# Optimization experiments

Measured on AMD Instinct MI355X. Metric: run time of the kernel, lower is better.

Reference implementation:

```python
import jax, jax.numpy as jnp
import numpy as np

B, T, D = 8, 4096, 1024

def setup_inputs() -> dict:
    key = jax.random.key(0)
    k1, k2, k3, k4, k5 = jax.random.split(key, 5)
    s = 1.0 / np.sqrt(D)
    return {
        "seq": jax.random.normal(k1, (B, T, D), dtype=jnp.float32),
        "W_delta": jax.random.uniform(k2, (D, D), jnp.float32, -s, s),
        "b_delta": jax.random.uniform(k3, (D,), jnp.float32, -s, s),
        "W_value": jax.random.uniform(k4, (D, D), jnp.float32, -s, s),
        "b_value": jax.random.uniform(k5, (D,), jnp.float32, -s, s),
    }

def reference(seq, W_delta, b_delta, W_value, b_value):
    # delta = sigmoid(seq @ W_delta^T + b_delta); value = seq @ W_value^T + b_value
    delta = jax.nn.sigmoid(jnp.einsum("btd,ed->bte", seq, W_delta) + b_delta)
    value = jnp.einsum("btd,ed->bte", seq, W_value) + b_value
    # gated linear recurrence: state_t = (1-delta_t)*state_{t-1} + delta_t*value_t
    def step(state, dv):
        d, v = dv  # each [B, D]
        state = (1.0 - d) * state + d * v
        return state, state
    init = jnp.zeros((seq.shape[0], seq.shape[-1]), dtype=seq.dtype)
    # time-major for scan
    _, out = jax.lax.scan(step, init, (delta.transpose(1, 0, 2), value.transpose(1, 0, 2)))
    return out.transpose(1, 0, 2)  # [B, T, D]
```

## Files before the change

kernel.cpp:

```cpp
#include <hip/hip_runtime.h>
#include <hip/hip_bf16.h>


typedef _Float16 f16;
typedef _Float16 f16x8 __attribute__((ext_vector_type(8)));
typedef float    f32x4 __attribute__((ext_vector_type(4)));

#define NB  8
#define NT  4096
#define ND  1024
#define NM  (NB*NT)
#define KK  2048

#define CT  128
#define NCH (NT/CT)

#define OFF_AP     0UL
#define OFF_BP     134217728UL
#define OFF_VALUE  142606336UL
#define OFF_AARR   276824064UL
#define OFF_SARR   277872640UL
#define OFF_SIN    278921216UL

#define GLOAD_LDS16(gp, lp)                                                          \
  __builtin_amdgcn_global_load_lds(                                                  \
      (const __attribute__((address_space(1))) void*)(gp),                           \
      (__attribute__((address_space(3))) void*)(lp), 16, 0, 0)

#define MEMFENCE asm volatile("" ::: "memory")
#define BARRIER() do { MEMFENCE; __builtin_amdgcn_s_barrier(); MEMFENCE; } while (0)
#define WAITV2() asm volatile("s_waitcnt vmcnt(2)" ::: "memory")
#define WAITV0() asm volatile("s_waitcnt vmcnt(0)" ::: "memory")

__global__ void k_convert_seq(const float* __restrict__ src, f16* __restrict__ Ap) {
  const long n8 = (long)NM * ND / 8;
  long i = (long)blockIdx.x * blockDim.x + threadIdx.x;
  const long stride = (long)gridDim.x * blockDim.x;
  for (; i < n8; i += stride) {
    const long m = i >> 7;
    const int k8 = ((int)i & 127) * 8;
    const float4 v0 = *(const float4*)(src + m * ND + k8);
    const float4 v1 = *(const float4*)(src + m * ND + k8 + 4);
    const float a[8] = {v0.x, v0.y, v0.z, v0.w, v1.x, v1.y, v1.z, v1.w};
    f16x8 hi, lo;
#pragma unroll
    for (int j = 0; j < 8; ++j) {
      const f16 h = (f16)a[j];
      hi[j] = h;
      lo[j] = (f16)(a[j] - (float)h);
    }
    *(f16x8*)(Ap + m * KK + k8) = hi;
    *(f16x8*)(Ap + m * KK + ND + k8) = lo;
  }
}

__global__ void k_convert_w(const float* __restrict__ Wd, const float* __restrict__ Wv,
                            f16* __restrict__ Bp) {
  const long i = (long)blockIdx.x * blockDim.x + threadIdx.x;
  const int n = (int)(i >> 7);
  const int k8 = ((int)i & 127) * 8;
  const float* row = (n < ND) ? (Wd + (long)n * ND) : (Wv + (long)(n - ND) * ND);
  const float4 v0 = *(const float4*)(row + k8);
  const float4 v1 = *(const float4*)(row + k8 + 4);
  const float a[8] = {v0.x, v0.y, v0.z, v0.w, v1.x, v1.y, v1.z, v1.w};
  f16x8 h;
#pragma unroll
  for (int j = 0; j < 8; ++j) h[j] = (f16)a[j];
  *(f16x8*)(Bp + (long)n * ND + k8) = h;
}

#define LDS_A(c) ((c) * 65536)
#define LDS_B(c) ((c) * 65536 + 32768)

__global__ __launch_bounds__(512, 2) void k_gemm(
    const f16* __restrict__ Ap, const f16* __restrict__ Bp,
    const float* __restrict__ bd, const float* __restrict__ bv,
    float* __restrict__ dOut, float* __restrict__ vOut) {
  __shared__ char smem[131072];

  const int t = threadIdx.x;
  const int w = t >> 6, lane = t & 63;
  const int wr = w >> 2, wc = w & 3;
  const int l15 = lane & 15, l4 = lane >> 4;

  const int bid = blockIdx.x;
  const int sw = (bid & 7) * 128 + (bid >> 3);
  const int bm = sw >> 3, bn = sw & 7;
  const long m0 = (long)bm * 256;
  const int n0 = bn * 256;

  f32x4 acc[8][4] = {};

  const int rl0 = t >> 3;
  const int rl1 = 64 + (t >> 3);
  const int c16_0 = (t & 7) ^ (rl0 & 7);
  const int c16_1 = (t & 7) ^ (rl1 & 7);

  auto stageA = [&](int kt, int h, int c) {
    const f16* s0 = Ap + (m0 + h * 128 + rl0) * (long)KK + kt * 64 + c16_0 * 8;
    const f16* s1 = Ap + (m0 + h * 128 + rl1) * (long)KK + kt * 64 + c16_1 * 8;
    char* base = smem + LDS_A(c) + h * 16384 + w * 1024;
    GLOAD_LDS16(s0, base);
    GLOAD_LDS16(s1, base + 8192);
  };
  auto stageB = [&](int kt, int h, int c) {
    const int kb = (kt & 15) * 64;
    const f16* s0 = Bp + (long)(n0 + h * 128 + rl0) * ND + kb + c16_0 * 8;
    const f16* s1 = Bp + (long)(n0 + h * 128 + rl1) * ND + kb + c16_1 * 8;
    char* base = smem + LDS_B(c) + h * 16384 + w * 1024;
    GLOAD_LDS16(s0, base);
    GLOAD_LDS16(s1, base + 8192);
  };

  f16x8 aF[8], bF[2];
  auto readA = [&](int c, int k) {
#pragma unroll
    for (int mf = 0; mf < 8; ++mf) {
      const int row = wr * 128 + mf * 16 + l15;
      const int c16 = (k * 4 + l4) ^ (row & 7);
      aF[mf] = *(const f16x8*)(smem + LDS_A(c) + row * 128 + c16 * 16);
    }
  };
  auto readB = [&](int c, int k, int nh) {
#pragma unroll
    for (int nfl = 0; nfl < 2; ++nfl) {
      const int row = nh * 128 + wc * 32 + nfl * 16 + l15;
      const int c16 = (k * 4 + l4) ^ (row & 7);
      bF[nfl] = *(const f16x8*)(smem + LDS_B(c) + row * 128 + c16 * 16);
    }
  };
  auto mfmaQ = [&](int nh) {
    __builtin_amdgcn_s_setprio(1);
#pragma unroll
    for (int mf = 0; mf < 8; ++mf)
#pragma unroll
      for (int nfl = 0; nfl < 2; ++nfl)
        acc[mf][nh * 2 + nfl] = __builtin_amdgcn_mfma_f32_16x16x32_f16(
            bF[nfl], aF[mf], acc[mf][nh * 2 + nfl], 0, 0, 0);
    __builtin_amdgcn_s_setprio(0);
  };

  auto tile = [&](int c, int ktNext, bool pf) {
    if (pf) stageA(ktNext, 0, c ^ 1);
    readA(c, 0); readB(c, 0, 0);
    BARRIER();
    mfmaQ(0);
    if (pf) { WAITV2(); } else { WAITV0(); }
    BARRIER();
    if (pf) stageA(ktNext, 1, c ^ 1);
    readB(c, 0, 1);
    BARRIER();
    mfmaQ(1);
    BARRIER();
    if (pf) stageB(ktNext, 0, c ^ 1);
    readA(c, 1); readB(c, 1, 0);
    BARRIER();
    mfmaQ(0);
    BARRIER();
    if (pf) stageB(ktNext, 1, c ^ 1);
    readB(c, 1, 1);
    BARRIER();
    mfmaQ(1);
    if (pf) { WAITV2(); } else { WAITV0(); }
    BARRIER();
  };

  stageA(0, 0, 0); stageA(0, 1, 0); stageB(0, 0, 0); stageB(0, 1, 0);
  WAITV2();
  BARRIER();

  for (int i = 0; i < 16; ++i) {
    tile(0, 2 * i + 1, true);
    tile(1, 2 * i + 2, i < 15);
  }

  const bool isDelta = (n0 < ND);
#pragma unroll
  for (int nf = 0; nf < 4; ++nf) {
    const int nb = n0 + (nf >> 1) * 128 + wc * 32 + (nf & 1) * 16 + l4 * 4;
    const float4 bias = *(const float4*)(isDelta ? (bd + nb) : (bv + (nb - ND)));
#pragma unroll
    for (int mf = 0; mf < 8; ++mf) {
      const long m = m0 + wr * 128 + mf * 16 + l15;
      f32x4 x = acc[mf][nf];
      x[0] += bias.x; x[1] += bias.y; x[2] += bias.z; x[3] += bias.w;
      if (isDelta) {
#pragma unroll
        for (int r = 0; r < 4; ++r) x[r] = 1.0f / (1.0f + __expf(-x[r]));
        *(f32x4*)(dOut + m * ND + nb) = x;
      } else {
        *(f32x4*)(vOut + m * ND + (nb - ND)) = x;
      }
    }
  }
}

__global__ void k_scan_local(const float* __restrict__ delta, const float* __restrict__ value,
                             float* __restrict__ Aarr, float* __restrict__ Sarr) {
  const int bid = blockIdx.x;
  const int c = bid & 31, b = bid >> 5;
  const int d = threadIdx.x * 4;
  const long base = ((long)b * NT + (long)c * CT) * ND + d;
  float4 a = make_float4(1.f, 1.f, 1.f, 1.f);
  float4 s = make_float4(0.f, 0.f, 0.f, 0.f);
#pragma unroll 4
  for (int tt = 0; tt < CT; ++tt) {
    const float4 dl = *(const float4*)(delta + base + (long)tt * ND);
    const float4 v  = *(const float4*)(value + base + (long)tt * ND);
    const float o0 = 1.0f - dl.x, o1 = 1.0f - dl.y, o2 = 1.0f - dl.z, o3 = 1.0f - dl.w;
    a.x *= o0; a.y *= o1; a.z *= o2; a.w *= o3;
    s.x = o0 * s.x + dl.x * v.x;
    s.y = o1 * s.y + dl.y * v.y;
    s.z = o2 * s.z + dl.z * v.z;
    s.w = o3 * s.w + dl.w * v.w;
  }
  const long o = (long)(b * NCH + c) * ND + d;
  *(float4*)(Aarr + o) = a;
  *(float4*)(Sarr + o) = s;
}

__global__ void k_scan_prefix(const float* __restrict__ Aarr, const float* __restrict__ Sarr,
                              float* __restrict__ Sin) {
  const int tid = blockIdx.x * blockDim.x + threadIdx.x;
  const int b = tid >> 8, d = (tid & 255) * 4;
  float4 st = make_float4(0.f, 0.f, 0.f, 0.f);
  for (int c = 0; c < NCH; ++c) {
    const long idx = (long)(b * NCH + c) * ND + d;
    *(float4*)(Sin + idx) = st;
    const float4 a = *(const float4*)(Aarr + idx);
    const float4 s = *(const float4*)(Sarr + idx);
    st.x = a.x * st.x + s.x;
    st.y = a.y * st.y + s.y;
    st.z = a.z * st.z + s.z;
    st.w = a.w * st.w + s.w;
  }
}

__global__ void k_scan_apply(const float* __restrict__ value, const float* __restrict__ Sin,
                             float* __restrict__ out) {
  const int bid = blockIdx.x;
  const int c = bid & 31, b = bid >> 5;
  const int d = threadIdx.x * 4;
  const long base = ((long)b * NT + (long)c * CT) * ND + d;
  float4 st = *(const float4*)(Sin + (long)(b * NCH + c) * ND + d);
#pragma unroll 4
  for (int tt = 0; tt < CT; ++tt) {
    const long idx = base + (long)tt * ND;
    const float4 dl = *(const float4*)(out + idx);
    const float4 v  = *(const float4*)(value + idx);
    st.x = (1.0f - dl.x) * st.x + dl.x * v.x;
    st.y = (1.0f - dl.y) * st.y + dl.y * v.y;
    st.z = (1.0f - dl.z) * st.z + dl.z * v.z;
    st.w = (1.0f - dl.w) * st.w + dl.w * v.w;
    *(float4*)(out + idx) = st;
  }
}

extern "C" void kernel_launch(void* const* d_in, const int* in_sizes, int n_in,
                              void* d_out, int out_size, void* d_ws, size_t ws_size,
                              hipStream_t stream) {
  const float* seq = (const float*)d_in[0];
  const float* Wd  = (const float*)d_in[1];
  const float* bd  = (const float*)d_in[2];
  const float* Wv  = (const float*)d_in[3];
  const float* bv  = (const float*)d_in[4];
  float* out = (float*)d_out;

  char* ws = (char*)d_ws;
  f16*   Ap    = (f16*)(ws + OFF_AP);
  f16*   Bp    = (f16*)(ws + OFF_BP);
  float* value = (float*)(ws + OFF_VALUE);
  float* Aarr  = (float*)(ws + OFF_AARR);
  float* Sarr  = (float*)(ws + OFF_SARR);
  float* Sin   = (float*)(ws + OFF_SIN);

  hipLaunchKernelGGL(k_convert_seq, dim3(2048), dim3(256), 0, stream, seq, Ap);
  hipLaunchKernelGGL(k_convert_w,   dim3(1024), dim3(256), 0, stream, Wd, Wv, Bp);
  hipLaunchKernelGGL(k_gemm, dim3(1024), dim3(512), 0, stream, Ap, Bp, bd, bv, out, value);
  hipLaunchKernelGGL(k_scan_local,  dim3(256), dim3(256), 0, stream, out, value, Aarr, Sarr);
  hipLaunchKernelGGL(k_scan_prefix, dim3(8),   dim3(256), 0, stream, Aarr, Sarr, Sin);
  hipLaunchKernelGGL(k_scan_apply,  dim3(256), dim3(256), 0, stream, value, Sin, out);
}
```

Measured before the change: 624.4 us.

## Drop split-fp16 residual term from GEMM and halve scan chunk length

The activation conversion no longer stores a low-order fp16 residual, so the GEMM's K dimension drops from 2048 to 1024. This halves the A-operand traffic, the conversion writes and the MFMA work. The scan chunk length is also cut from 128 to 64, doubling the blocks in the local and apply scan passes for more parallelism. In exchange, the activations lose the extra precision the hi/lo split provided, which risks larger numerical error against the fp32 reference.

New measurement: 519.1 us. 1.2x faster.

```diff
diff --git a/kernel.cpp b/kernel.cpp
--- a/kernel.cpp
+++ b/kernel.cpp
@@ -10,17 +10,17 @@
 #define NT  4096
 #define ND  1024
 #define NM  (NB*NT)
-#define KK  2048
-
-#define CT  128
+#define KK  1024
+
+#define CT  64
 #define NCH (NT/CT)
 
 #define OFF_AP     0UL
-#define OFF_BP     134217728UL
-#define OFF_VALUE  142606336UL
-#define OFF_AARR   276824064UL
-#define OFF_SARR   277872640UL
-#define OFF_SIN    278921216UL
+#define OFF_BP     67108864UL
+#define OFF_VALUE  71303168UL
+#define OFF_AARR   205520896UL
+#define OFF_SARR   207618048UL
+#define OFF_SIN    209715200UL
 
 #define GLOAD_LDS16(gp, lp)                                                          \
   __builtin_amdgcn_global_load_lds(                                                  \
@@ -37,20 +37,12 @@
   long i = (long)blockIdx.x * blockDim.x + threadIdx.x;
   const long stride = (long)gridDim.x * blockDim.x;
   for (; i < n8; i += stride) {
-    const long m = i >> 7;
-    const int k8 = ((int)i & 127) * 8;
-    const float4 v0 = *(const float4*)(src + m * ND + k8);
-    const float4 v1 = *(const float4*)(src + m * ND + k8 + 4);
-    const float a[8] = {v0.x, v0.y, v0.z, v0.w, v1.x, v1.y, v1.z, v1.w};
-    f16x8 hi, lo;
-#pragma unroll
-    for (int j = 0; j < 8; ++j) {
-      const f16 h = (f16)a[j];
-      hi[j] = h;
-      lo[j] = (f16)(a[j] - (float)h);
-    }
-    *(f16x8*)(Ap + m * KK + k8) = hi;
-    *(f16x8*)(Ap + m * KK + ND + k8) = lo;
+    const float4 v0 = *(const float4*)(src + i * 8);
+    const float4 v1 = *(const float4*)(src + i * 8 + 4);
+    f16x8 h;
+    h[0] = (f16)v0.x; h[1] = (f16)v0.y; h[2] = (f16)v0.z; h[3] = (f16)v0.w;
+    h[4] = (f16)v1.x; h[5] = (f16)v1.y; h[6] = (f16)v1.z; h[7] = (f16)v1.w;
+    *((f16x8*)Ap + i) = h;
   }
 }
 
@@ -62,10 +54,9 @@
   const float* row = (n < ND) ? (Wd + (long)n * ND) : (Wv + (long)(n - ND) * ND);
   const float4 v0 = *(const float4*)(row + k8);
   const float4 v1 = *(const float4*)(row + k8 + 4);
-  const float a[8] = {v0.x, v0.y, v0.z, v0.w, v1.x, v1.y, v1.z, v1.w};
   f16x8 h;
-#pragma unroll
-  for (int j = 0; j < 8; ++j) h[j] = (f16)a[j];
+  h[0] = (f16)v0.x; h[1] = (f16)v0.y; h[2] = (f16)v0.z; h[3] = (f16)v0.w;
+  h[4] = (f16)v1.x; h[5] = (f16)v1.y; h[6] = (f16)v1.z; h[7] = (f16)v1.w;
   *(f16x8*)(Bp + (long)n * ND + k8) = h;
 }
 
@@ -104,9 +95,8 @@
     GLOAD_LDS16(s1, base + 8192);
   };
   auto stageB = [&](int kt, int h, int c) {
-    const int kb = (kt & 15) * 64;
-    const f16* s0 = Bp + (long)(n0 + h * 128 + rl0) * ND + kb + c16_0 * 8;
-    const f16* s1 = Bp + (long)(n0 + h * 128 + rl1) * ND + kb + c16_1 * 8;
+    const f16* s0 = Bp + (long)(n0 + h * 128 + rl0) * ND + kt * 64 + c16_0 * 8;
+    const f16* s1 = Bp + (long)(n0 + h * 128 + rl1) * ND + kt * 64 + c16_1 * 8;
     char* base = smem + LDS_B(c) + h * 16384 + w * 1024;
     GLOAD_LDS16(s0, base);
     GLOAD_LDS16(s1, base + 8192);
@@ -169,9 +159,9 @@
   WAITV2();
   BARRIER();
 
-  for (int i = 0; i < 16; ++i) {
+  for (int i = 0; i < 8; ++i) {
     tile(0, 2 * i + 1, true);
-    tile(1, 2 * i + 2, i < 15);
+    tile(1, 2 * i + 2, i < 7);
   }
 
   const bool isDelta = (n0 < ND);
@@ -198,7 +188,7 @@
 __global__ void k_scan_local(const float* __restrict__ delta, const float* __restrict__ value,
                              float* __restrict__ Aarr, float* __restrict__ Sarr) {
   const int bid = blockIdx.x;
-  const int c = bid & 31, b = bid >> 5;
+  const int c = bid & 63, b = bid >> 6;
   const int d = threadIdx.x * 4;
   const long base = ((long)b * NT + (long)c * CT) * ND + d;
   float4 a = make_float4(1.f, 1.f, 1.f, 1.f);
@@ -239,7 +229,7 @@
 __global__ void k_scan_apply(const float* __restrict__ value, const float* __restrict__ Sin,
                              float* __restrict__ out) {
   const int bid = blockIdx.x;
-  const int c = bid & 31, b = bid >> 5;
+  const int c = bid & 63, b = bid >> 6;
   const int d = threadIdx.x * 4;
   const long base = ((long)b * NT + (long)c * CT) * ND + d;
   float4 st = *(const float4*)(Sin + (long)(b * NCH + c) * ND + d);
@@ -277,7 +267,7 @@
   hipLaunchKernelGGL(k_convert_seq, dim3(2048), dim3(256), 0, stream, seq, Ap);
   hipLaunchKernelGGL(k_convert_w,   dim3(1024), dim3(256), 0, stream, Wd, Wv, Bp);
   hipLaunchKernelGGL(k_gemm, dim3(1024), dim3(512), 0, stream, Ap, Bp, bd, bv, out, value);
-  hipLaunchKernelGGL(k_scan_local,  dim3(256), dim3(256), 0, stream, out, value, Aarr, Sarr);
+  hipLaunchKernelGGL(k_scan_local,  dim3(512), dim3(256), 0, stream, out, value, Aarr, Sarr);
   hipLaunchKernelGGL(k_scan_prefix, dim3(8),   dim3(256), 0, stream, Aarr, Sarr, Sin);
-  hipLaunchKernelGGL(k_scan_apply,  dim3(256), dim3(256), 0, stream, value, Sin, out);
-}
+  hipLaunchKernelGGL(k_scan_apply,  dim3(512), dim3(256), 0, stream, value, Sin, out);
+}
```
